# Optimization experiments

Measured on AMD Instinct MI355X. Metric: run time of the kernel, lower is better.

Reference implementation:

```python
import jax, jax.numpy as jnp
import numpy as np
from jax import lax

SPATIAL = 4
DN = ('NCHW', 'OIHW', 'NCHW')

def setup_inputs() -> dict:
    key = jax.random.key(0)
    ks = jax.random.split(key, 6)
    b, c_in, h, w = 32, 256, 56, 56
    c_out, kk, n_exp, red = 256, 3, 3, 16
    fan = c_in * kk * kk
    return {
        'x': jax.random.normal(ks[0], (b, c_in, h, w), jnp.float32),
        'w_expert': jax.random.normal(ks[1], (n_exp, c_out, c_in, kk, kk), jnp.float32) / np.sqrt(fan),
        'route_conv_w': jax.random.normal(ks[2], (red, c_in), jnp.float32) / np.sqrt(c_in),
        'route_conv_b': jax.random.normal(ks[3], (red,), jnp.float32) * 0.05,
        'fc_w': jax.random.normal(ks[4], (n_exp, red * SPATIAL * SPATIAL), jnp.float32) / np.sqrt(red * SPATIAL * SPATIAL),
        'fc_b': jax.random.normal(ks[5], (n_exp,), jnp.float32) * 0.05,
    }

def _routing(x, route_conv_w, route_conv_b, fc_w, fc_b):
    b, c, h, w = x.shape
    # AdaptiveAvgPool2d(4): h, w divisible by 4 -> exact block mean
    pooled = x.reshape(b, c, SPATIAL, h // SPATIAL, SPATIAL, w // SPATIAL).mean(axis=(3, 5))  # [b,c,4,4]
    r = jnp.einsum('bcij,rc->brij', pooled, route_conv_w) + route_conv_b[None, :, None, None]
    r = jax.nn.relu(r).reshape(b, -1)                         # [b, red*16]
    r = jax.nn.relu(r @ fc_w.T + fc_b)                        # [b, n_exp]
    return jax.nn.sigmoid(r)

def reference(x, w_expert, route_conv_w, route_conv_b, fc_w, fc_b):
    rw = _routing(x, route_conv_w, route_conv_b, fc_w, fc_b)              # [b,k]
    cw = jnp.einsum('bk,koihw->boihw', rw, w_expert)                      # per-sample mixed weights
    def conv1(xi, wi):
        return lax.conv_general_dilated(xi[None], wi, window_strides=(1, 1),
                                        padding=[(1, 1), (1, 1)],
                                        dimension_numbers=DN)[0]
    return jax.vmap(conv1)(x, cw)  # [b, c_out, h, w]
```

## Files before the change

kernel.cpp:

```cpp
#include <hip/hip_runtime.h>
#include <hip/hip_bf16.h>
#include <stdint.h>

#define NB   32
#define CIN  256
#define COUT 256
#define WW   56
#define HW   3136
#define NEXP 3
#define KTOT 2304
#define XP   58
#define XPP  3364
#define NKT  36

typedef __attribute__((ext_vector_type(8))) __bf16 bf16x8;
typedef __attribute__((ext_vector_type(4))) float  f32x4;

#define OFF_RW     0
#define OFF_POOLED 1024
#define OFF_CWT    (1024 + 32*256*16*4)
#define CWT_BYTES  ((size_t)NB*COUT*KTOT*2)
#define OFF_XPAD   (OFF_CWT + CWT_BYTES)

#define PRE_XPAD 6272
#define PRE_POOL 8192
#define PRE_NBLK (PRE_XPAD + PRE_POOL + NB)

__global__ __launch_bounds__(256) void k_pre(const float* __restrict__ x,
                                             float* __restrict__ pooled,
                                             __bf16* __restrict__ xpad) {
    __shared__ __align__(16) char smem[8448];
    int blk = blockIdx.x;
    int t = threadIdx.x;

    if (blk < PRE_XPAD) {
        int pt = blk % 49;
        int r2 = blk / 49;
        int ct = r2 & 3;
        int b  = r2 >> 2;
        __bf16 (*lds)[66] = (__bf16(*)[66])smem;
        int pl = t & 63;
        int cb = t >> 6;
        const float* xb = x + ((size_t)(b * CIN + ct * 64)) * HW + pt * 64;
        #pragma unroll
        for (int ic = 0; ic < 16; ++ic) {
            int cl = ic * 4 + cb;
            lds[cl][pl] = (__bf16)xb[(size_t)cl * HW + pl];
        }
        __syncthreads();
        #pragma unroll
        for (int iw = 0; iw < 2; ++iw) {
            int idx = iw * 256 + t;
            int p_l = idx >> 3, c8 = (idx & 7) * 8;
            int p = pt * 64 + p_l;
            int y = p / WW, xx = p - y * WW;
            union { __bf16 h[8]; uint4 u; } pk;
            #pragma unroll
            for (int j = 0; j < 8; ++j) pk.h[j] = lds[c8 + j][p_l];
            __bf16* dst = xpad + ((size_t)b * XPP + (y + 1) * XP + (xx + 1)) * CIN
                          + ct * 64 + c8;
            *(uint4*)dst = pk.u;
        }
    } else if (blk < PRE_XPAD + PRE_POOL) {
        int j = blk - PRE_XPAD;
        int b = j >> 8, c = j & 255;
        float (*lds)[56] = (float(*)[56])smem;
        const float* xb = x + ((size_t)(b * CIN + c)) * HW;
        if (t < 224) {
            int xc = t % 56, yg = t / 56;
            const float* p = xb + (yg * 14) * WW + xc;
            float s = 0.f;
            #pragma unroll
            for (int r = 0; r < 14; ++r) s += p[r * WW];
            lds[yg][xc] = s;
        }
        __syncthreads();
        if (t < 16) {
            int sy = t >> 2, sx = t & 3;
            float s = 0.f;
            #pragma unroll
            for (int jj = 0; jj < 14; ++jj) s += lds[sy][sx * 14 + jj];
            pooled[(((size_t)b * CIN + c) << 4) + t] = s * (1.f / 196.f);
        }
    } else {
        int b = blk - (PRE_XPAD + PRE_POOL);
        for (int idx = t; idx < 228 * 32; idx += 256) {
            int pos = idx >> 5;
            int co = (idx & 31) * 8;
            int yy, xx;
            if (pos < 58)       { yy = 0;          xx = pos; }
            else if (pos < 116) { yy = 57;         xx = pos - 58; }
            else if (pos < 172) { yy = pos - 115;  xx = 0; }
            else                { yy = pos - 171;  xx = 57; }
            uint4 z = {0u, 0u, 0u, 0u};
            *(uint4*)(xpad + ((size_t)b * XPP + yy * XP + xx) * CIN + co) = z;
        }
    }
}

__global__ __launch_bounds__(256) void k_route(const float* __restrict__ pooled,
                                               const float* __restrict__ rcw,
                                               const float* __restrict__ rcb,
                                               const float* __restrict__ fcw,
                                               const float* __restrict__ fcb,
                                               float* __restrict__ rw) {
    int b = blockIdx.x;
    int t = threadIdx.x;
    int r = t >> 4, ij = t & 15;
    __shared__ float rbuf[256];
    const float* pb = pooled + (size_t)b * CIN * 16;
    float acc = rcb[r];
    for (int c = 0; c < CIN; ++c)
        acc += pb[c * 16 + ij] * rcw[r * CIN + c];
    rbuf[t] = fmaxf(acc, 0.f);
    __syncthreads();
    if (t < NEXP) {
        float a = fcb[t];
        for (int f = 0; f < 256; ++f) a += rbuf[f] * fcw[t * 256 + f];
        a = fmaxf(a, 0.f);
        rw[b * NEXP + t] = 1.f / (1.f + expf(-a));
    }
}

__global__ __launch_bounds__(256) void k_mixw(const float* __restrict__ we,
                                              const float* __restrict__ rw,
                                              __bf16* __restrict__ cwt) {
    int o = blockIdx.x;
    int i = threadIdx.x;
    float wv[3][9];
    #pragma unroll
    for (int e = 0; e < 3; ++e) {
        const float* p = we + (((size_t)e * COUT + o) * CIN + i) * 9;
        #pragma unroll
        for (int k = 0; k < 9; ++k) wv[e][k] = p[k];
    }
    for (int b = 0; b < NB; ++b) {
        float r0 = rw[b * 3 + 0], r1 = rw[b * 3 + 1], r2 = rw[b * 3 + 2];
        __bf16* op = cwt + ((size_t)(b * COUT + o)) * KTOT + i;
        #pragma unroll
        for (int k = 0; k < 9; ++k) {
            float v = r0 * wv[0][k] + r1 * wv[1][k] + r2 * wv[2][k];
            op[k * 256] = (__bf16)v;
        }
    }
}

#define GL16(g, l) __builtin_amdgcn_global_load_lds( \
    (const __attribute__((address_space(1))) uint32_t*)(g), \
    (__attribute__((address_space(3))) uint32_t*)(l), 16, 0, 0)

#define STAGE_A(o, kh, aoffn) \
    GL16(gA + (aoffn) + (kh)*64, LDS + (o)*32768 + (kh)*16384 + wid*1024)
#define STAGE_B(o, kh, boffn) \
    GL16(gB + (boffn) + (kh)*64, LDS + 65536 + (o)*32768 + (kh)*16384 + wid*1024)

#define BARRIER() do { \
    __builtin_amdgcn_sched_barrier(0); \
    __builtin_amdgcn_s_barrier(); \
    __builtin_amdgcn_sched_barrier(0); \
  } while (0)
#define VMCNT(n) do { \
    asm volatile("s_waitcnt vmcnt(" #n ")" ::: "memory"); \
    __builtin_amdgcn_sched_barrier(0); \
  } while (0)
#define LGKM0() do { \
    asm volatile("s_waitcnt lgkmcnt(0)" ::: "memory"); \
    __builtin_amdgcn_sched_barrier(0); \
  } while (0)

#define LOAD4(F, base) do { \
    F[0] = *(const bf16x8*)((base) + 0); \
    F[1] = *(const bf16x8*)((base) + 1024); \
    F[2] = *(const bf16x8*)((base) + 2048); \
    F[3] = *(const bf16x8*)((base) + 3072); \
  } while (0)
#define MMALL() do { \
    __builtin_amdgcn_s_setprio(1); \
    _Pragma("unroll") \
    for (int mf = 0; mf < 4; ++mf) \
      _Pragma("unroll") \
      for (int nf = 0; nf < 4; ++nf) \
        acc[mf][nf] = __builtin_amdgcn_mfma_f32_16x16x32_bf16( \
            af[mf], bq[nf], acc[mf][nf], 0, 0, 0); \
    __builtin_amdgcn_s_setprio(0); \
  } while (0)

#define PHASE(c, o, kh, aoffn, boffn) do { \
    { const char* aCur = LDS + (c)*32768 + (kh)*16384 + aRd; \
      const char* bCur = LDS + 65536 + (c)*32768 + (kh)*16384 + bRd; \
      LOAD4(af, aCur); \
      LOAD4(bq, bCur); } \
    STAGE_A(o, kh, aoffn); \
    STAGE_B(o, kh, boffn); \
    VMCNT(2); \
    BARRIER(); \
    LGKM0(); \
    MMALL(); \
  } while (0)

__global__ __launch_bounds__(1024, 4) void k_conv(const __bf16* __restrict__ cwt,
                                                  const __bf16* __restrict__ xpad,
                                                  float* __restrict__ out) {
    extern __shared__ __align__(16) char LDS[];

    int flat = blockIdx.x;
    int logical = (flat & 7) * 52 + (flat >> 3);
    int b  = logical / 13;
    int nt = logical - b * 13;

    int tid = threadIdx.x;
    int ln  = tid & 63;
    int wid = tid >> 6;
    int wr  = wid >> 2;
    int wc  = wid & 3;
    int fr  = ln & 15;
    int kw  = ln >> 4;
    int xsw = ((fr >> 1) & 3) << 4;

    const char *gA, *gB;
    {
        const char* cwb = (const char*)(cwt + (size_t)b * COUT * KTOT);
        const char* xpb = (const char*)(xpad + (size_t)b * XPP * CIN);
        int L = tid * 16;
        int U = L ^ (((L >> 7) & 3) << 4);
        int rowU = U >> 6;
        int kbU  = U & 63;
        gA = cwb + (size_t)rowU * (KTOT * 2) + kbU;
        int p = nt * 256 + rowU; if (p > HW - 1) p = HW - 1;
        int y = p / WW, x = p - y * WW;
        gB = xpb + (size_t)(y * XP + x) * (CIN * 2) + kbU;
    }

    int aRd = (wr * 64 + fr) * 64 + ((kw * 16) ^ xsw);
    int bRd = (wc * 64 + fr) * 64 + ((kw * 16) ^ xsw);

    f32x4 acc[4][4];
    #pragma unroll
    for (int i = 0; i < 4; ++i)
        #pragma unroll
        for (int j = 0; j < 4; ++j)
            acc[i][j] = (f32x4){0.f, 0.f, 0.f, 0.f};

    bf16x8 af[4], bq[4];

    STAGE_A(0, 0, 0);
    STAGE_B(0, 0, 0);
    STAGE_A(0, 1, 0);
    STAGE_B(0, 1, 0);
    VMCNT(2);
    BARRIER();

    for (int kt = 0; kt < NKT - 1; ++kt) {
        int c = kt & 1, o = c ^ 1;
        int ktn  = kt + 1;
        int aoffn = ktn * 128;
        int ktap = ktn >> 2;
        int kyn  = (ktap * 11) >> 5;
        int kxn  = ktap - kyn * 3;
        int boffn = (kyn * XP + kxn) * 512 + (ktn & 3) * 128;

        PHASE(c, o, 0, aoffn, boffn);
        PHASE(c, o, 1, aoffn, boffn);
    }

    {
        const char* aCur = LDS + 32768 + aRd;
        const char* bCur = LDS + 65536 + 32768 + bRd;
        LOAD4(af, aCur); LOAD4(bq, bCur);
        VMCNT(0);
        BARRIER();
        LGKM0();
        MMALL();
        aCur += 16384; bCur += 16384;
        LOAD4(af, aCur); LOAD4(bq, bCur);
        LGKM0();
        MMALL();
    }

    float* ob = out + ((size_t)(b * COUT + wr * 64)) * HW;
    int colbase = nt * 256 + wc * 64;
    int rb = (ln >> 4) * 4;
    #pragma unroll
    for (int nf = 0; nf < 4; ++nf) {
        int col = colbase + nf * 16 + fr;
        if (col < HW) {
            #pragma unroll
            for (int mf = 0; mf < 4; ++mf)
                #pragma unroll
                for (int r = 0; r < 4; ++r)
                    ob[(size_t)(mf * 16 + rb + r) * HW + col] = acc[mf][nf][r];
        }
    }
}

extern "C" void kernel_launch(void* const* d_in, const int* in_sizes, int n_in,
                              void* d_out, int out_size, void* d_ws, size_t ws_size,
                              hipStream_t stream) {
    (void)in_sizes; (void)n_in; (void)out_size; (void)ws_size;
    const float* x   = (const float*)d_in[0];
    const float* we  = (const float*)d_in[1];
    const float* rcw = (const float*)d_in[2];
    const float* rcb = (const float*)d_in[3];
    const float* fcw = (const float*)d_in[4];
    const float* fcb = (const float*)d_in[5];
    float* out = (float*)d_out;

    char* ws = (char*)d_ws;
    float*  rw     = (float*)(ws + OFF_RW);
    float*  pooled = (float*)(ws + OFF_POOLED);
    __bf16* cwt    = (__bf16*)(ws + OFF_CWT);
    __bf16* xpad   = (__bf16*)(ws + OFF_XPAD);

    (void)hipFuncSetAttribute((const void*)k_conv,
                              hipFuncAttributeMaxDynamicSharedMemorySize, 131072);

    k_pre<<<PRE_NBLK, 256, 0, stream>>>(x, pooled, xpad);
    k_route<<<NB, 256, 0, stream>>>(pooled, rcw, rcb, fcw, fcb, rw);
    k_mixw<<<COUT, 256, 0, stream>>>(we, rw, cwt);
    k_conv<<<416, 1024, 131072, stream>>>(cwt, xpad, out);
}
```

Baseline: 195.1 us.

## Load conv B operand directly from global into registers, bypassing LDS

The activation (B) tiles are no longer staged through LDS. Each lane now loads its MFMA B fragments straight from global memory into double-buffered registers, one half-tile ahead, while only the weight (A) tiles still go through LDS. This halves LDS use to 64KB and removes the LDS write/read traffic for B. In exchange, the same B data is read redundantly by the four wave rows from global/L2, and the vmcnt waits are retuned to the new mix of direct and LDS-bound loads.

```diff
diff --git a/kernel.cpp b/kernel.cpp
--- a/kernel.cpp
+++ b/kernel.cpp
@@ -149,10 +149,8 @@
     (const __attribute__((address_space(1))) uint32_t*)(g), \
     (__attribute__((address_space(3))) uint32_t*)(l), 16, 0, 0)
 
-#define STAGE_A(o, kh, aoffn) \
-    GL16(gA + (aoffn) + (kh)*64, LDS + (o)*32768 + (kh)*16384 + wid*1024)
-#define STAGE_B(o, kh, boffn) \
-    GL16(gB + (boffn) + (kh)*64, LDS + 65536 + (o)*32768 + (kh)*16384 + wid*1024)
+#define STAGE_A(o, h, aoffn) \
+    GL16(gA + (aoffn) + (h)*64, LDS + (o)*32768 + (h)*16384 + tid*16)
 
 #define BARRIER() do { \
     __builtin_amdgcn_sched_barrier(0); \
@@ -168,34 +166,28 @@
     __builtin_amdgcn_sched_barrier(0); \
   } while (0)
 
-#define LOAD4(F, base) do { \
-    F[0] = *(const bf16x8*)((base) + 0); \
-    F[1] = *(const bf16x8*)((base) + 1024); \
-    F[2] = *(const bf16x8*)((base) + 2048); \
-    F[3] = *(const bf16x8*)((base) + 3072); \
-  } while (0)
-#define MMALL() do { \
+#define LOADA(c, h) do { \
+    const char* aCur = LDS + (c)*32768 + (h)*16384 + aRd; \
+    af[0] = *(const bf16x8*)(aCur + 0); \
+    af[1] = *(const bf16x8*)(aCur + 1024); \
+    af[2] = *(const bf16x8*)(aCur + 2048); \
+    af[3] = *(const bf16x8*)(aCur + 3072); \
+  } while (0)
+#define BLOAD(S, boff) do { \
+    S[0] = *(const bf16x8*)(bP0 + (boff)); \
+    S[1] = *(const bf16x8*)(bP1 + (boff)); \
+    S[2] = *(const bf16x8*)(bP2 + (boff)); \
+    S[3] = *(const bf16x8*)(bP3 + (boff)); \
+  } while (0)
+#define MM(S) do { \
     __builtin_amdgcn_s_setprio(1); \
     _Pragma("unroll") \
     for (int mf = 0; mf < 4; ++mf) \
       _Pragma("unroll") \
       for (int nf = 0; nf < 4; ++nf) \
         acc[mf][nf] = __builtin_amdgcn_mfma_f32_16x16x32_bf16( \
-            af[mf], bq[nf], acc[mf][nf], 0, 0, 0); \
+            af[mf], S[nf], acc[mf][nf], 0, 0, 0); \
     __builtin_amdgcn_s_setprio(0); \
-  } while (0)
-
-#define PHASE(c, o, kh, aoffn, boffn) do { \
-    { const char* aCur = LDS + (c)*32768 + (kh)*16384 + aRd; \
-      const char* bCur = LDS + 65536 + (c)*32768 + (kh)*16384 + bRd; \
-      LOAD4(af, aCur); \
-      LOAD4(bq, bCur); } \
-    STAGE_A(o, kh, aoffn); \
-    STAGE_B(o, kh, boffn); \
-    VMCNT(2); \
-    BARRIER(); \
-    LGKM0(); \
-    MMALL(); \
   } while (0)
 
 __global__ __launch_bounds__(1024, 4) void k_conv(const __bf16* __restrict__ cwt,
@@ -217,22 +209,30 @@
     int kw  = ln >> 4;
     int xsw = ((fr >> 1) & 3) << 4;
 
-    const char *gA, *gB;
+    const char* gA;
     {
         const char* cwb = (const char*)(cwt + (size_t)b * COUT * KTOT);
-        const char* xpb = (const char*)(xpad + (size_t)b * XPP * CIN);
         int L = tid * 16;
         int U = L ^ (((L >> 7) & 3) << 4);
         int rowU = U >> 6;
         int kbU  = U & 63;
         gA = cwb + (size_t)rowU * (KTOT * 2) + kbU;
-        int p = nt * 256 + rowU; if (p > HW - 1) p = HW - 1;
-        int y = p / WW, x = p - y * WW;
-        gB = xpb + (size_t)(y * XP + x) * (CIN * 2) + kbU;
+    }
+    const char *bP0, *bP1, *bP2, *bP3;
+    {
+        const char* xpb = (const char*)(xpad + (size_t)b * XPP * CIN);
+        #pragma unroll
+        for (int nf = 0; nf < 4; ++nf) {
+            int p = nt * 256 + wc * 64 + nf * 16 + fr;
+            if (p > HW - 1) p = HW - 1;
+            int y = p / WW, x = p - y * WW;
+            const char* bp = xpb + (size_t)(y * XP + x) * (CIN * 2) + kw * 16;
+            if (nf == 0) bP0 = bp; else if (nf == 1) bP1 = bp;
+            else if (nf == 2) bP2 = bp; else bP3 = bp;
+        }
     }
 
     int aRd = (wr * 64 + fr) * 64 + ((kw * 16) ^ xsw);
-    int bRd = (wc * 64 + fr) * 64 + ((kw * 16) ^ xsw);
 
     f32x4 acc[4][4];
     #pragma unroll
@@ -241,40 +241,55 @@
         for (int j = 0; j < 4; ++j)
             acc[i][j] = (f32x4){0.f, 0.f, 0.f, 0.f};
 
-    bf16x8 af[4], bq[4];
-
+    bf16x8 af[4], bqA[4], bqB[4];
+
+    BLOAD(bqA, 0);
     STAGE_A(0, 0, 0);
-    STAGE_B(0, 0, 0);
     STAGE_A(0, 1, 0);
-    STAGE_B(0, 1, 0);
-    VMCNT(2);
+    VMCNT(1);
     BARRIER();
 
     for (int kt = 0; kt < NKT - 1; ++kt) {
         int c = kt & 1, o = c ^ 1;
+        int tap  = kt >> 2;
+        int ky   = (tap * 11) >> 5;
+        int kx   = tap - ky * 3;
+        int boff_h1 = (ky * XP + kx) * 512 + (kt & 3) * 128 + 64;
         int ktn  = kt + 1;
+        int tapn = ktn >> 2;
+        int kyn  = (tapn * 11) >> 5;
+        int kxn  = tapn - kyn * 3;
+        int boff_n0 = (kyn * XP + kxn) * 512 + (ktn & 3) * 128;
         int aoffn = ktn * 128;
-        int ktap = ktn >> 2;
-        int kyn  = (ktap * 11) >> 5;
-        int kxn  = ktap - kyn * 3;
-        int boffn = (kyn * XP + kxn) * 512 + (ktn & 3) * 128;
-
-        PHASE(c, o, 0, aoffn, boffn);
-        PHASE(c, o, 1, aoffn, boffn);
-    }
-
-    {
-        const char* aCur = LDS + 32768 + aRd;
-        const char* bCur = LDS + 65536 + 32768 + bRd;
-        LOAD4(af, aCur); LOAD4(bq, bCur);
-        VMCNT(0);
+
+        BLOAD(bqB, boff_h1);
+        STAGE_A(o, 0, aoffn);
+        LOADA(c, 0);
+        VMCNT(5);
         BARRIER();
         LGKM0();
-        MMALL();
-        aCur += 16384; bCur += 16384;
-        LOAD4(af, aCur); LOAD4(bq, bCur);
+        MM(bqA);
+        BLOAD(bqA, boff_n0);
+        STAGE_A(o, 1, aoffn);
+        LOADA(c, 1);
+        VMCNT(5);
+        BARRIER();
         LGKM0();
-        MMALL();
+        MM(bqB);
+    }
+
+    {
+        const int boff_35_1 = (2 * XP + 2) * 512 + 3 * 128 + 64;
+        BLOAD(bqB, boff_35_1);
+        LOADA(1, 0);
+        VMCNT(4);
+        BARRIER();
+        LGKM0();
+        MM(bqA);
+        LOADA(1, 1);
+        VMCNT(0);
+        LGKM0();
+        MM(bqB);
     }
 
     float* ob = out + ((size_t)(b * COUT + wr * 64)) * HW;
@@ -312,10 +327,10 @@
     __bf16* xpad   = (__bf16*)(ws + OFF_XPAD);
 
     (void)hipFuncSetAttribute((const void*)k_conv,
-                              hipFuncAttributeMaxDynamicSharedMemorySize, 131072);
+                              hipFuncAttributeMaxDynamicSharedMemorySize, 65536);
 
     k_pre<<<PRE_NBLK, 256, 0, stream>>>(x, pooled, xpad);
     k_route<<<NB, 256, 0, stream>>>(pooled, rcw, rcb, fcw, fcb, rw);
     k_mixw<<<COUT, 256, 0, stream>>>(we, rw, cwt);
-    k_conv<<<416, 1024, 131072, stream>>>(cwt, xpad, out);
-}
+    k_conv<<<416, 1024, 65536, stream>>>(cwt, xpad, out);
+}
```

New measurement: 362.2 us. 85.7% more time.

## Retile implicit-GEMM conv to 128x448 blocks with 8 waves and 7 N-fragments

Applied to the files above, without the earlier changes.

Changes the conv block tile from 256x256 (16 waves) to 128 output channels by 448 pixels (8 waves). Each wave now computes 64x112 with 28 MFMAs per k-step, so it reuses the A fragments more and performs fewer LDS reads per MFMA. Since 3136 = 7x448, the pixel tail is gone and the column bounds check is dropped. In exchange it uses more LDS (about 148KB), needs an odd B staging split across waves, and holds more accumulator registers, which lowers occupancy.

```diff
diff --git a/kernel.cpp b/kernel.cpp
--- a/kernel.cpp
+++ b/kernel.cpp
@@ -149,64 +149,74 @@
     (const __attribute__((address_space(1))) uint32_t*)(g), \
     (__attribute__((address_space(3))) uint32_t*)(l), 16, 0, 0)
 
-#define STAGE_A(o, kh, aoffn) \
-    GL16(gA + (aoffn) + (kh)*64, LDS + (o)*32768 + (kh)*16384 + wid*1024)
-#define STAGE_B(o, kh, boffn) \
-    GL16(gB + (boffn) + (kh)*64, LDS + 65536 + (o)*32768 + (kh)*16384 + wid*1024)
-
-#define BARRIER() do { \
-    __builtin_amdgcn_sched_barrier(0); \
-    __builtin_amdgcn_s_barrier(); \
-    __builtin_amdgcn_sched_barrier(0); \
-  } while (0)
+#define SB0() __builtin_amdgcn_sched_barrier(0)
+#define BARRIER() do { SB0(); __builtin_amdgcn_s_barrier(); SB0(); } while (0)
 #define VMCNT(n) do { \
-    asm volatile("s_waitcnt vmcnt(" #n ")" ::: "memory"); \
-    __builtin_amdgcn_sched_barrier(0); \
+    asm volatile("s_waitcnt vmcnt(" #n ")" ::: "memory"); SB0(); \
   } while (0)
 #define LGKM0() do { \
-    asm volatile("s_waitcnt lgkmcnt(0)" ::: "memory"); \
-    __builtin_amdgcn_sched_barrier(0); \
-  } while (0)
-
-#define LOAD4(F, base) do { \
-    F[0] = *(const bf16x8*)((base) + 0); \
-    F[1] = *(const bf16x8*)((base) + 1024); \
-    F[2] = *(const bf16x8*)((base) + 2048); \
-    F[3] = *(const bf16x8*)((base) + 3072); \
-  } while (0)
-#define MMALL() do { \
+    asm volatile("s_waitcnt lgkmcnt(0)" ::: "memory"); SB0(); \
+  } while (0)
+
+#define STAGE(o, kh, aoffn, boffn) do { \
+    GL16(gA + (aoffn) + (kh)*64, LDS + (o)*16384 + (kh)*8192 + wid*1024); \
+    GL16(gB0 + (boffn) + (kh)*64, \
+         LDS + 32768 + (o)*57344 + (kh)*28672 + 0    + wid*1024); \
+    GL16(gB1 + (boffn) + (kh)*64, \
+         LDS + 32768 + (o)*57344 + (kh)*28672 + 8192 + wid*1024); \
+    GL16(gB2 + (boffn) + (kh)*64, \
+         LDS + 32768 + (o)*57344 + (kh)*28672 + 16384 + wid*1024); \
+    GL16(gB3 + (boffn) + (kh)*64, ldsB3dst + (o)*57344 + (kh)*28672); \
+  } while (0)
+
+#define READF(c, kh) do { \
+    const char* aCur = LDS + (c)*16384 + (kh)*8192 + aRd; \
+    const char* bCur = LDS + 32768 + (c)*57344 + (kh)*28672 + bRd; \
+    af[0] = *(const bf16x8*)(aCur + 0); \
+    af[1] = *(const bf16x8*)(aCur + 1024); \
+    af[2] = *(const bf16x8*)(aCur + 2048); \
+    af[3] = *(const bf16x8*)(aCur + 3072); \
+    bq[0] = *(const bf16x8*)(bCur + 0); \
+    bq[1] = *(const bf16x8*)(bCur + 1024); \
+    bq[2] = *(const bf16x8*)(bCur + 2048); \
+    bq[3] = *(const bf16x8*)(bCur + 3072); \
+    bq[4] = *(const bf16x8*)(bCur + 4096); \
+    bq[5] = *(const bf16x8*)(bCur + 5120); \
+    bq[6] = *(const bf16x8*)(bCur + 6144); \
+    SB0(); \
+  } while (0)
+
+#define MM28() do { \
     __builtin_amdgcn_s_setprio(1); \
     _Pragma("unroll") \
     for (int mf = 0; mf < 4; ++mf) \
       _Pragma("unroll") \
-      for (int nf = 0; nf < 4; ++nf) \
+      for (int nf = 0; nf < 7; ++nf) \
         acc[mf][nf] = __builtin_amdgcn_mfma_f32_16x16x32_bf16( \
             af[mf], bq[nf], acc[mf][nf], 0, 0, 0); \
     __builtin_amdgcn_s_setprio(0); \
   } while (0)
 
 #define PHASE(c, o, kh, aoffn, boffn) do { \
-    { const char* aCur = LDS + (c)*32768 + (kh)*16384 + aRd; \
-      const char* bCur = LDS + 65536 + (c)*32768 + (kh)*16384 + bRd; \
-      LOAD4(af, aCur); \
-      LOAD4(bq, bCur); } \
-    STAGE_A(o, kh, aoffn); \
-    STAGE_B(o, kh, boffn); \
-    VMCNT(2); \
+    READF(c, kh); \
+    STAGE(o, kh, aoffn, boffn); \
+    VMCNT(5); \
     BARRIER(); \
     LGKM0(); \
-    MMALL(); \
-  } while (0)
-
-__global__ __launch_bounds__(1024, 4) void k_conv(const __bf16* __restrict__ cwt,
-                                                  const __bf16* __restrict__ xpad,
-                                                  float* __restrict__ out) {
+    MM28(); \
+  } while (0)
+
+__global__ __launch_bounds__(512, 2) void k_conv(const __bf16* __restrict__ cwt,
+                                                 const __bf16* __restrict__ xpad,
+                                                 float* __restrict__ out) {
     extern __shared__ __align__(16) char LDS[];
 
     int flat = blockIdx.x;
-    int logical = (flat & 7) * 52 + (flat >> 3);
-    int b  = logical / 13;
-    int nt = logical - b * 13;
+    int logical = (flat & 7) * 56 + (flat >> 3);
+    int b   = logical / 14;
+    int rem = logical - b * 14;
+    int mtile = rem / 7;
+    int ntile = rem - mtile * 7;
 
     int tid = threadIdx.x;
     int ln  = tid & 63;
@@ -217,37 +227,55 @@
     int kw  = ln >> 4;
     int xsw = ((fr >> 1) & 3) << 4;
 
-    const char *gA, *gB;
+    const char *gA, *gB0, *gB1, *gB2, *gB3;
+    char* ldsB3dst;
     {
         const char* cwb = (const char*)(cwt + (size_t)b * COUT * KTOT);
         const char* xpb = (const char*)(xpad + (size_t)b * XPP * CIN);
-        int L = tid * 16;
-        int U = L ^ (((L >> 7) & 3) << 4);
-        int rowU = U >> 6;
-        int kbU  = U & 63;
-        gA = cwb + (size_t)rowU * (KTOT * 2) + kbU;
-        int p = nt * 256 + rowU; if (p > HW - 1) p = HW - 1;
-        int y = p / WW, x = p - y * WW;
-        gB = xpb + (size_t)(y * XP + x) * (CIN * 2) + kbU;
+        {
+            int L = tid * 16;
+            int U = L ^ (((L >> 7) & 3) << 4);
+            int rowU = U >> 6;
+            int kbU  = U & 63;
+            gA = cwb + (size_t)(mtile * 128 + rowU) * (KTOT * 2) + kbU;
+        }
+        #pragma unroll
+        for (int c = 0; c < 4; ++c) {
+            int L = c * 8192 + tid * 16;
+            int U = L ^ (((L >> 7) & 3) << 4);
+            int rowU = U >> 6;
+            int kbU  = U & 63;
+            const char* gb;
+            if (rowU < 448) {
+                int p = ntile * 448 + rowU;
+                int y = p / WW, x = p - y * WW;
+                gb = xpb + (size_t)(y * XP + x) * (CIN * 2) + kbU;
+            } else {
+                gb = xpb + kbU;
+            }
+            if (c == 0) gB0 = gb; else if (c == 1) gB1 = gb;
+            else if (c == 2) gB2 = gb; else gB3 = gb;
+        }
+        ldsB3dst = (wid < 4)
+                 ? (LDS + 32768 + 24576 + wid * 1024)
+                 : (LDS + 147456 + (wid - 4) * 1024);
     }
 
     int aRd = (wr * 64 + fr) * 64 + ((kw * 16) ^ xsw);
-    int bRd = (wc * 64 + fr) * 64 + ((kw * 16) ^ xsw);
-
-    f32x4 acc[4][4];
+    int bRd = (wc * 112 + fr) * 64 + ((kw * 16) ^ xsw);
+
+    f32x4 acc[4][7];
     #pragma unroll
     for (int i = 0; i < 4; ++i)
         #pragma unroll
-        for (int j = 0; j < 4; ++j)
+        for (int j = 0; j < 7; ++j)
             acc[i][j] = (f32x4){0.f, 0.f, 0.f, 0.f};
 
-    bf16x8 af[4], bq[4];
-
-    STAGE_A(0, 0, 0);
-    STAGE_B(0, 0, 0);
-    STAGE_A(0, 1, 0);
-    STAGE_B(0, 1, 0);
-    VMCNT(2);
+    bf16x8 af[4], bq[7];
+
+    STAGE(0, 0, 0, 0);
+    STAGE(0, 1, 0, 0);
+    VMCNT(5);
     BARRIER();
 
     for (int kt = 0; kt < NKT - 1; ++kt) {
@@ -264,32 +292,27 @@
     }
 
     {
-        const char* aCur = LDS + 32768 + aRd;
-        const char* bCur = LDS + 65536 + 32768 + bRd;
-        LOAD4(af, aCur); LOAD4(bq, bCur);
+        READF(1, 0);
         VMCNT(0);
         BARRIER();
         LGKM0();
-        MMALL();
-        aCur += 16384; bCur += 16384;
-        LOAD4(af, aCur); LOAD4(bq, bCur);
+        MM28();
+        READF(1, 1);
         LGKM0();
-        MMALL();
-    }
-
-    float* ob = out + ((size_t)(b * COUT + wr * 64)) * HW;
-    int colbase = nt * 256 + wc * 64;
+        MM28();
+    }
+
+    float* ob = out + ((size_t)(b * COUT + mtile * 128 + wr * 64)) * HW;
+    int colbase = ntile * 448 + wc * 112;
     int rb = (ln >> 4) * 4;
     #pragma unroll
-    for (int nf = 0; nf < 4; ++nf) {
+    for (int nf = 0; nf < 7; ++nf) {
         int col = colbase + nf * 16 + fr;
-        if (col < HW) {
+        #pragma unroll
+        for (int mf = 0; mf < 4; ++mf)
             #pragma unroll
-            for (int mf = 0; mf < 4; ++mf)
-                #pragma unroll
-                for (int r = 0; r < 4; ++r)
-                    ob[(size_t)(mf * 16 + rb + r) * HW + col] = acc[mf][nf][r];
-        }
+            for (int r = 0; r < 4; ++r)
+                ob[(size_t)(mf * 16 + rb + r) * HW + col] = acc[mf][nf][r];
     }
 }
 
@@ -312,10 +335,10 @@
     __bf16* xpad   = (__bf16*)(ws + OFF_XPAD);
 
     (void)hipFuncSetAttribute((const void*)k_conv,
-                              hipFuncAttributeMaxDynamicSharedMemorySize, 131072);
+                              hipFuncAttributeMaxDynamicSharedMemorySize, 151552);
 
     k_pre<<<PRE_NBLK, 256, 0, stream>>>(x, pooled, xpad);
     k_route<<<NB, 256, 0, stream>>>(pooled, rcw, rcb, fcw, fcb, rw);
     k_mixw<<<COUT, 256, 0, stream>>>(we, rw, cwt);
-    k_conv<<<416, 1024, 131072, stream>>>(cwt, xpad, out);
-}
+    k_conv<<<448, 512, 151552, stream>>>(cwt, xpad, out);
+}
```

Result: no change. 194.4 us (-0.3%).
